# Performance work log

Hardware: AMD Instinct MI355X
Metric: run time of the kernel (lower is better)

## Reference

```python
import jax, jax.numpy as jnp
import numpy as np


def crf_log_likelihood(logits, tags, mask, transitions, start_trans, end_trans):
    """AllenNLP-style linear-chain CRF log-likelihood, summed over the batch.
    logits: [B,T,K] float, tags: [B,T] int, mask: [B,T] float (1=valid).
    include_start_end_transitions=True.
    """
    B, T, K = logits.shape
    lt = jnp.transpose(logits, (1, 0, 2))          # [T,B,K]
    mt = jnp.transpose(mask, (1, 0))               # [T,B]
    tt = jnp.transpose(tags, (1, 0))               # [T,B]

    # ---- partition function (forward algorithm) ----
    alpha0 = start_trans + lt[0]                   # [B,K]

    def part_step(alpha, xs):
        emit, m = xs                               # emit [B,K], m [B]
        # inner[b,i,j] = alpha[b,i] + transitions[i,j] + emit[b,j]
        inner = alpha[:, :, None] + emit[:, None, :] + transitions[None, :, :]
        new_alpha = jax.nn.logsumexp(inner, axis=1)
        alpha = new_alpha * m[:, None] + alpha * (1.0 - m[:, None])
        return alpha, None

    alpha, _ = jax.lax.scan(part_step, alpha0, (lt[1:], mt[1:]))
    log_denominator = jax.nn.logsumexp(alpha + end_trans, axis=1)  # [B]

    # ---- joint (gold-path) score ----
    score0 = start_trans[tt[0]]                    # [B]

    def joint_step(score, xs):
        cur, nxt, emit, m_cur, m_nxt = xs
        trans_s = transitions[cur, nxt]                                   # [B]
        emit_s = jnp.take_along_axis(emit, cur[:, None], axis=1)[:, 0]    # [B]
        return score + trans_s * m_nxt + emit_s * m_cur, None

    score, _ = jax.lax.scan(joint_step, score0,
                            (tt[:-1], tt[1:], lt[:-1], mt[:-1], mt[1:]))
    last_idx = (jnp.sum(mt, axis=0) - 1.0).astype(jnp.int32)              # [B]
    last_tags = tt[last_idx, jnp.arange(B)]                               # [B]
    last_emit = jnp.take_along_axis(lt[-1], last_tags[:, None], axis=1)[:, 0]
    score = score + end_trans[last_tags] + last_emit * mt[-1]
    return jnp.sum(score - log_denominator)


def setup_inputs() -> dict:
    key = jax.random.key(0)
    ks = jax.random.split(key, 6)
    B, T, D, K = 64, 512, 768, 21
    vectors = jax.random.normal(ks[0], (B, T, D), dtype=jnp.float32)
    targets = jax.random.randint(ks[1], (B, T), 0, K, dtype=jnp.int32)
    mask = jnp.ones((B, T), dtype=jnp.int32)
    # Linear(input_dim, n_classes)
    W = jax.random.normal(ks[2], (K, D), dtype=jnp.float32) * (1.0 / np.sqrt(D))
    b = jax.random.normal(ks[3], (K,), dtype=jnp.float32) * 0.01
    transitions = jax.random.normal(ks[4], (K, K), dtype=jnp.float32) * 0.1
    se = jax.random.normal(ks[5], (2, K), dtype=jnp.float32) * 0.1
    return {"vectors": vectors, "targets": targets, "mask": mask,
            "W": W, "b": b, "transitions": transitions,
            "start_trans": se[0], "end_trans": se[1]}


def reference(vectors, targets, mask, W, b, transitions, start_trans, end_trans):
    logits = jnp.einsum('btd,kd->btk', vectors, W) + b     # proj
    maskf = mask.astype(logits.dtype)
    ll = crf_log_likelihood(logits, targets, maskf, transitions, start_trans, end_trans)
    loss = -ll / jnp.sum(maskf)
    return loss, logits
```

## Files before the change

### kernel.cpp

```cpp
#include <hip/hip_runtime.h>

#define B_ 64
#define T_ 512
#define D_ 768
#define K_ 21
#define NCHUNK 32
#define CLEN 16
#define GSTRIDE 448
#define LOG21 3.0445224377234229965f

__global__ __launch_bounds__(512) void proj_kernel(
    const float* __restrict__ A,
    const float* __restrict__ W,
    const float* __restrict__ bias,
    float* __restrict__ out)
{
    __shared__ float Wl[K_ * D_];
    const int tid = threadIdx.x;
    {
        const float4* Wg = (const float4*)W;
        float4* Ws = (float4*)Wl;
        for (int i = tid; i < K_ * D_ / 4; i += 512) Ws[i] = Wg[i];
    }
    __syncthreads();

    const int m = tid & 15;
    const size_t row = (size_t)blockIdx.x * 32 + (tid >> 4);
    const float4* __restrict__ Arow = (const float4*)(A + row * D_);
    const float4* __restrict__ Wl4 = (const float4*)Wl;

    float acc[K_];
    #pragma unroll
    for (int k = 0; k < K_; ++k) acc[k] = 0.0f;

    #pragma unroll 4
    for (int i = 0; i < 12; ++i) {
        const float4 a = Arow[m + 16 * i];
        #pragma unroll
        for (int k = 0; k < K_; ++k) {
            const float4 w = Wl4[k * 192 + m + 16 * i];
            acc[k] = fmaf(a.x, w.x, fmaf(a.y, w.y, fmaf(a.z, w.z, fmaf(a.w, w.w, acc[k]))));
        }
    }

    #pragma unroll
    for (int k = 0; k < K_; ++k) {
        float v = acc[k];
        v += __shfl_xor(v, 1, 64);
        v += __shfl_xor(v, 2, 64);
        v += __shfl_xor(v, 4, 64);
        v += __shfl_xor(v, 8, 64);
        acc[k] = v;
    }

    float* o = out + 1 + row * K_;
    #pragma unroll
    for (int k = 0; k < K_; ++k) {
        if (m == (k & 15)) o[k] = acc[k] + bias[k];
    }
}

__global__ __launch_bounds__(64) void chunk_kernel(
    const float* __restrict__ outF,
    const int*   __restrict__ mask,
    const float* __restrict__ trans,
    float* __restrict__ G,
    float* __restrict__ SC)
{
    __shared__ float M0[441], M1[441];
    __shared__ float sET[441];
    __shared__ float em[CLEN * K_];
    __shared__ float smx[CLEN];
    __shared__ int   smask[CLEN];

    const int c = blockIdx.x;
    const int b = blockIdx.y;
    const int lane = threadIdx.x;
    const int t0 = c * CLEN + 1;
    const int nst = min(CLEN, T_ - t0);
    const int i_ = lane / 3;
    const int jg = lane - i_ * 3;
    const bool act = lane < 63;

    const float* lg = outF + 1 + (size_t)b * T_ * K_;
    for (int idx = lane; idx < nst * K_; idx += 64) em[idx] = lg[t0 * K_ + idx];
    if (lane < nst) smask[lane] = mask[b * T_ + t0 + lane];
    for (int idx = lane; idx < 441; idx += 64) {
        M0[idx] = (idx % 22 == 0) ? 1.0f : 0.0f;
        sET[idx] = __expf(trans[idx]);
    }
    __syncthreads();

    if (lane < nst) {
        float mx = -1e30f;
        for (int j = 0; j < K_; ++j) mx = fmaxf(mx, em[lane * K_ + j]);
        smx[lane] = mx;
    }
    __syncthreads();
    for (int idx = lane; idx < nst * K_; idx += 64)
        em[idx] = __expf(em[idx] - smx[idx / K_]) * (1.0f / 21.0f);

    float ETc[K_ * 7];
    if (act) {
        #pragma unroll
        for (int mm = 0; mm < K_; ++mm) {
            #pragma unroll
            for (int q = 0; q < 7; ++q)
                ETc[mm * 7 + q] = sET[mm * K_ + jg * 7 + q];
        }
    }
    __syncthreads();

    int cur = 0;
    for (int s = 0; s < nst; ++s) {
        if (smask[s] != 0) {
            const float* Mr = cur ? M1 : M0;
            float*       Mw = cur ? M0 : M1;
            float facc[7] = {0.f,0.f,0.f,0.f,0.f,0.f,0.f};
            if (act) {
                #pragma unroll
                for (int mm = 0; mm < K_; ++mm) {
                    const float lm = Mr[i_ * K_ + mm];
                    #pragma unroll
                    for (int q = 0; q < 7; ++q)
                        facc[q] = fmaf(lm, ETc[mm * 7 + q], facc[q]);
                }
            }
            __syncthreads();
            if (act) {
                #pragma unroll
                for (int q = 0; q < 7; ++q)
                    Mw[i_ * K_ + jg * 7 + q] = facc[q] * em[s * K_ + jg * 7 + q];
            }
            __syncthreads();
            cur ^= 1;
        }
    }

    float* Gc = G + (size_t)(b * NCHUNK + c) * GSTRIDE;
    const float* Mf = cur ? M1 : M0;
    for (int idx = lane; idx < 441; idx += 64) Gc[idx] = Mf[idx];
    if (lane == 0) {
        float sc = 0.0f;
        for (int s = 0; s < nst; ++s)
            if (smask[s] != 0) sc += smx[s] + LOG21;
        SC[b * NCHUNK + c] = sc;
    }
}

__global__ __launch_bounds__(64) void scan_kernel(
    const float* __restrict__ outF,
    const int*   __restrict__ tags,
    const int*   __restrict__ mask,
    const float* __restrict__ trans,
    const float* __restrict__ startT,
    const float* __restrict__ endT,
    const float* __restrict__ G,
    const float* __restrict__ SC,
    float* __restrict__ ll,
    float* __restrict__ msum)
{
    __shared__ float sG[2][GSTRIDE];
    __shared__ float sv[24];
    __shared__ float sm[T_];
    __shared__ int   st[T_];
    const int b = blockIdx.x;
    const int lane = threadIdx.x;
    const int jc = min(lane, K_ - 1);
    const float* lg = outF + 1 + (size_t)b * T_ * K_;
    const float* Gb = G + (size_t)b * NCHUNK * GSTRIDE;

    for (int t = lane; t < T_; t += 64) {
        sm[t] = (float)mask[b * T_ + t];
        st[t] = tags[b * T_ + t];
    }
    const float scv = (lane < NCHUNK) ? SC[b * NCHUNK + lane] : 0.0f;

    {
        const float4* Gf4 = (const float4*)Gb;
        float4* dst = (float4*)sG[0];
        dst[lane] = Gf4[lane];
        if (lane < 48) dst[lane + 64] = Gf4[lane + 64];
    }

    float val = (lane < K_) ? startT[lane] + lg[lane] : -1e30f;
    float mx = val;
    #pragma unroll
    for (int off = 32; off >= 1; off >>= 1) mx = fmaxf(mx, __shfl_xor(mx, off, 64));
    float v = (lane < K_) ? __expf(val - mx) : 0.0f;
    float C = mx;

    for (int c = 0; c < NCHUNK; ++c) {
        if (lane < K_) sv[lane] = v;
        __syncthreads();

        float4 p0, p1;
        const bool have = (c + 1) < NCHUNK;
        if (have) {
            const float4* Gf4 = (const float4*)(Gb + (size_t)(c + 1) * GSTRIDE);
            p0 = Gf4[lane];
            if (lane < 48) p1 = Gf4[lane + 64];
        }

        const float* Gc = sG[c & 1];
        float a0 = 0.f, a1 = 0.f, a2 = 0.f;
        #pragma unroll
        for (int i = 0; i < K_; i += 3) {
            a0 = fmaf(sv[i],     Gc[i * K_ + jc],       a0);
            a1 = fmaf(sv[i + 1], Gc[(i + 1) * K_ + jc], a1);
            a2 = fmaf(sv[i + 2], Gc[(i + 2) * K_ + jc], a2);
        }
        const float s = a0 + a1 + a2;
        C += __shfl(scv, c, 64);
        float m2 = (lane < K_) ? s : 0.0f;
        #pragma unroll
        for (int off = 32; off >= 1; off >>= 1) m2 = fmaxf(m2, __shfl_xor(m2, off, 64));
        v = (lane < K_) ? s / m2 : 0.0f;
        C += __logf(m2);

        if (have) {
            float4* dst = (float4*)sG[(c + 1) & 1];
            dst[lane] = p0;
            if (lane < 48) dst[lane + 64] = p1;
        }
        __syncthreads();
    }

    float term = (lane < K_) ? v * __expf(endT[lane]) : 0.0f;
    #pragma unroll
    for (int off = 32; off >= 1; off >>= 1) term += __shfl_xor(term, off, 64);
    const float logZ = C + __logf(term);

    float sc = 0.0f, ms = 0.0f;
    for (int t = lane; t < T_; t += 64) {
        const float mt = sm[t];
        ms += mt;
        if (t < T_ - 1) {
            const int ct = st[t], nt2 = st[t + 1];
            sc += trans[ct * K_ + nt2] * sm[t + 1] + lg[t * K_ + ct] * mt;
        }
    }
    #pragma unroll
    for (int off = 32; off >= 1; off >>= 1) {
        sc += __shfl_xor(sc, off, 64);
        ms += __shfl_xor(ms, off, 64);
    }
    if (lane == 0) {
        const int lastIdx = (int)ms - 1;
        const int lastTag = st[lastIdx];
        sc += startT[st[0]] + endT[lastTag] + lg[(T_ - 1) * K_ + lastTag] * sm[T_ - 1];
        ll[b]   = sc - logZ;
        msum[b] = ms;
    }
}

__global__ __launch_bounds__(64) void crf_kernel(
    const float* __restrict__ outF,
    const int*   __restrict__ tags,
    const int*   __restrict__ mask,
    const float* __restrict__ trans,
    const float* __restrict__ startT,
    const float* __restrict__ endT,
    float* __restrict__ ws)
{
    __shared__ float se[T_ * K_];
    __shared__ float sm[T_];
    __shared__ int   st[T_];
    const int b = blockIdx.x;
    const int lane = threadIdx.x;

    const float* lg = outF + 1 + (size_t)b * T_ * K_;
    for (int i = lane; i < T_ * K_; i += 64) se[i] = lg[i];
    for (int t = lane; t < T_; t += 64) {
        sm[t] = (float)mask[b * T_ + t];
        st[t] = tags[b * T_ + t];
    }
    __syncthreads();

    const int jc = lane < K_ ? lane : K_ - 1;
    float ET[K_];
    #pragma unroll
    for (int i = 0; i < K_; ++i) ET[i] = __expf(trans[i * K_ + jc]);

    float a0   = startT[jc] + se[jc];
    float r0   = __shfl(a0, 0, 64);
    float aRel = a0 - r0;
    float C    = r0;

    for (int t = 1; t < T_; ++t) {
        if (sm[t] != 0.0f) {
            float e = __expf(aRel);
            float s = 0.0f;
            #pragma unroll
            for (int i = 0; i < K_; ++i)
                s = fmaf(__shfl(e, i, 64), ET[i], s);
            float raw = __logf(s) + se[t * K_ + jc];
            float rr  = __shfl(raw, 0, 64);
            aRel = raw - rr;
            C   += rr;
        }
    }

    float contrib = (lane < K_) ? __expf(aRel + endT[jc]) : 0.0f;
    #pragma unroll
    for (int off = 32; off >= 1; off >>= 1) contrib += __shfl_xor(contrib, off, 64);
    const float logZ = C + __logf(contrib);

    float sc = 0.0f, ms = 0.0f;
    for (int t = lane; t < T_; t += 64) {
        const float mt = sm[t];
        ms += mt;
        if (t < T_ - 1) {
            const int ct = st[t], nt2 = st[t + 1];
            sc += trans[ct * K_ + nt2] * sm[t + 1] + se[t * K_ + ct] * mt;
        }
    }
    #pragma unroll
    for (int off = 32; off >= 1; off >>= 1) {
        sc += __shfl_xor(sc, off, 64);
        ms += __shfl_xor(ms, off, 64);
    }
    if (lane == 0) {
        const int lastIdx = (int)ms - 1;
        const int lastTag = st[lastIdx];
        sc += startT[st[0]] + endT[lastTag] + se[(T_ - 1) * K_ + lastTag] * sm[T_ - 1];
        ws[b]      = sc - logZ;
        ws[B_ + b] = ms;
    }
}

__global__ __launch_bounds__(64) void fin_kernel(
    const float* __restrict__ ll, const float* __restrict__ msum,
    float* __restrict__ outF)
{
    const int lane = threadIdx.x;
    float l = ll[lane];
    float m = msum[lane];
    #pragma unroll
    for (int off = 32; off >= 1; off >>= 1) {
        l += __shfl_xor(l, off, 64);
        m += __shfl_xor(m, off, 64);
    }
    if (lane == 0) outF[0] = -l / m;
}

extern "C" void kernel_launch(void* const* d_in, const int* in_sizes, int n_in,
                              void* d_out, int out_size, void* d_ws, size_t ws_size,
                              hipStream_t stream) {
    const float* A     = (const float*)d_in[0];
    const int*   tags  = (const int*)  d_in[1];
    const int*   mask  = (const int*)  d_in[2];
    const float* W     = (const float*)d_in[3];
    const float* bias  = (const float*)d_in[4];
    const float* trans = (const float*)d_in[5];
    const float* stT   = (const float*)d_in[6];
    const float* enT   = (const float*)d_in[7];
    float* outF = (float*)d_out;
    float* ws   = (float*)d_ws;

    proj_kernel<<<1024, 512, 0, stream>>>(A, W, bias, outF);

    const size_t gFloats  = (size_t)B_ * NCHUNK * GSTRIDE;
    const size_t scOff    = gFloats;
    const size_t llOff    = gFloats + (size_t)B_ * NCHUNK;
    const size_t msOff    = llOff + B_;
    const size_t needBytes = (msOff + B_) * sizeof(float);

    if (ws_size >= needBytes) {
        float* G   = ws;
        float* SC  = ws + scOff;
        float* llp = ws + llOff;
        float* msv = ws + msOff;
        chunk_kernel<<<dim3(NCHUNK, B_), 64, 0, stream>>>(outF, mask, trans, G, SC);
        scan_kernel<<<B_, 64, 0, stream>>>(outF, tags, mask, trans, stT, enT, G, SC, llp, msv);
        fin_kernel<<<1, 64, 0, stream>>>(llp, msv, outF);
    } else {
        crf_kernel<<<B_, 64, 0, stream>>>(outF, tags, mask, trans, stT, enT, ws);
        fin_kernel<<<1, 64, 0, stream>>>(ws, ws + B_, outF);
    }
}
```

Baseline: 218.3 us.

## Use fp16 MFMA for projection and preload all chunk matrices in scan

The projection kernel now computes the 32768x21 logits with fp16 MFMA 16x16x32 instructions. Each wave handles 16 rows and reads A and W directly from global memory, converting to half on the fly, instead of staging W in LDS and doing scalar FMAs with shuffle reductions. Separately, the scan kernel loads all 32 chunk transfer matrices into shared memory up front rather than double-buffering one chunk per iteration. This takes global loads off the serial scan loop. The cost is reduced logit precision from fp16 rounding of the inputs and a much larger LDS footprint per scan block.

```diff
diff --git a/kernel.cpp b/kernel.cpp
--- a/kernel.cpp
+++ b/kernel.cpp
@@ -9,54 +9,61 @@
 #define GSTRIDE 448
 #define LOG21 3.0445224377234229965f
 
-__global__ __launch_bounds__(512) void proj_kernel(
+using f16x8 = __attribute__((ext_vector_type(8))) _Float16;
+using f32x4 = __attribute__((ext_vector_type(4))) float;
+
+__global__ __launch_bounds__(256) void proj_kernel(
     const float* __restrict__ A,
     const float* __restrict__ W,
     const float* __restrict__ bias,
     float* __restrict__ out)
 {
-    __shared__ float Wl[K_ * D_];
-    const int tid = threadIdx.x;
+    const int lane = threadIdx.x & 63;
+    const int wave = threadIdx.x >> 6;
+    const int row0 = (blockIdx.x * 4 + wave) * 16;
+    const int m = lane & 15;
+    const int kb = (lane >> 4) * 8;
+
+    const float* __restrict__ Ar  = A + (size_t)(row0 + m) * D_ + kb;
+    const float* __restrict__ Wr0 = W + (size_t)m * D_ + kb;
+    const int n1 = (16 + m < K_) ? 16 + m : K_ - 1;
+    const float* __restrict__ Wr1 = W + (size_t)n1 * D_ + kb;
+
+    f32x4 acc0 = {0.f, 0.f, 0.f, 0.f};
+    f32x4 acc1 = {0.f, 0.f, 0.f, 0.f};
+
+    #pragma unroll 8
+    for (int s = 0; s < 24; ++s) {
+        const float4 aL = *(const float4*)(Ar  + s * 32);
+        const float4 aH = *(const float4*)(Ar  + s * 32 + 4);
+        const float4 bL = *(const float4*)(Wr0 + s * 32);
+        const float4 bH = *(const float4*)(Wr0 + s * 32 + 4);
+        const float4 cL = *(const float4*)(Wr1 + s * 32);
+        const float4 cH = *(const float4*)(Wr1 + s * 32 + 4);
+        f16x8 af, bf, cf;
+        af[0]=(_Float16)aL.x; af[1]=(_Float16)aL.y; af[2]=(_Float16)aL.z; af[3]=(_Float16)aL.w;
+        af[4]=(_Float16)aH.x; af[5]=(_Float16)aH.y; af[6]=(_Float16)aH.z; af[7]=(_Float16)aH.w;
+        bf[0]=(_Float16)bL.x; bf[1]=(_Float16)bL.y; bf[2]=(_Float16)bL.z; bf[3]=(_Float16)bL.w;
+        bf[4]=(_Float16)bH.x; bf[5]=(_Float16)bH.y; bf[6]=(_Float16)bH.z; bf[7]=(_Float16)bH.w;
+        cf[0]=(_Float16)cL.x; cf[1]=(_Float16)cL.y; cf[2]=(_Float16)cL.z; cf[3]=(_Float16)cL.w;
+        cf[4]=(_Float16)cH.x; cf[5]=(_Float16)cH.y; cf[6]=(_Float16)cH.z; cf[7]=(_Float16)cH.w;
+        acc0 = __builtin_amdgcn_mfma_f32_16x16x32_f16(af, bf, acc0, 0, 0, 0);
+        acc1 = __builtin_amdgcn_mfma_f32_16x16x32_f16(af, cf, acc1, 0, 0, 0);
+    }
+
+    const int rbase = row0 + (lane >> 4) * 4;
     {
-        const float4* Wg = (const float4*)W;
-        float4* Ws = (float4*)Wl;
-        for (int i = tid; i < K_ * D_ / 4; i += 512) Ws[i] = Wg[i];
-    }
-    __syncthreads();
-
-    const int m = tid & 15;
-    const size_t row = (size_t)blockIdx.x * 32 + (tid >> 4);
-    const float4* __restrict__ Arow = (const float4*)(A + row * D_);
-    const float4* __restrict__ Wl4 = (const float4*)Wl;
-
-    float acc[K_];
-    #pragma unroll
-    for (int k = 0; k < K_; ++k) acc[k] = 0.0f;
-
-    #pragma unroll 4
-    for (int i = 0; i < 12; ++i) {
-        const float4 a = Arow[m + 16 * i];
-        #pragma unroll
-        for (int k = 0; k < K_; ++k) {
-            const float4 w = Wl4[k * 192 + m + 16 * i];
-            acc[k] = fmaf(a.x, w.x, fmaf(a.y, w.y, fmaf(a.z, w.z, fmaf(a.w, w.w, acc[k]))));
-        }
-    }
-
-    #pragma unroll
-    for (int k = 0; k < K_; ++k) {
-        float v = acc[k];
-        v += __shfl_xor(v, 1, 64);
-        v += __shfl_xor(v, 2, 64);
-        v += __shfl_xor(v, 4, 64);
-        v += __shfl_xor(v, 8, 64);
-        acc[k] = v;
-    }
-
-    float* o = out + 1 + row * K_;
-    #pragma unroll
-    for (int k = 0; k < K_; ++k) {
-        if (m == (k & 15)) o[k] = acc[k] + bias[k];
+        const float bb = bias[m];
+        float* o = out + 1 + (size_t)rbase * K_ + m;
+        #pragma unroll
+        for (int r = 0; r < 4; ++r) o[(size_t)r * K_] = acc0[r] + bb;
+    }
+    const int col2 = 16 + m;
+    if (col2 < K_) {
+        const float bb = bias[col2];
+        float* o = out + 1 + (size_t)rbase * K_ + col2;
+        #pragma unroll
+        for (int r = 0; r < 4; ++r) o[(size_t)r * K_] = acc1[r] + bb;
     }
 }
 
@@ -160,7 +167,7 @@
     float* __restrict__ ll,
     float* __restrict__ msum)
 {
-    __shared__ float sG[2][GSTRIDE];
+    __shared__ float sG[NCHUNK * GSTRIDE];
     __shared__ float sv[24];
     __shared__ float sm[T_];
     __shared__ int   st[T_];
@@ -170,39 +177,29 @@
     const float* lg = outF + 1 + (size_t)b * T_ * K_;
     const float* Gb = G + (size_t)b * NCHUNK * GSTRIDE;
 
+    {
+        const float4* Gf4 = (const float4*)Gb;
+        float4* dst = (float4*)sG;
+        for (int j = lane; j < NCHUNK * GSTRIDE / 4; j += 64) dst[j] = Gf4[j];
+    }
     for (int t = lane; t < T_; t += 64) {
         sm[t] = (float)mask[b * T_ + t];
         st[t] = tags[b * T_ + t];
     }
     const float scv = (lane < NCHUNK) ? SC[b * NCHUNK + lane] : 0.0f;
 
-    {
-        const float4* Gf4 = (const float4*)Gb;
-        float4* dst = (float4*)sG[0];
-        dst[lane] = Gf4[lane];
-        if (lane < 48) dst[lane + 64] = Gf4[lane + 64];
-    }
-
     float val = (lane < K_) ? startT[lane] + lg[lane] : -1e30f;
     float mx = val;
     #pragma unroll
     for (int off = 32; off >= 1; off >>= 1) mx = fmaxf(mx, __shfl_xor(mx, off, 64));
     float v = (lane < K_) ? __expf(val - mx) : 0.0f;
     float C = mx;
+    __syncthreads();
 
     for (int c = 0; c < NCHUNK; ++c) {
         if (lane < K_) sv[lane] = v;
         __syncthreads();
-
-        float4 p0, p1;
-        const bool have = (c + 1) < NCHUNK;
-        if (have) {
-            const float4* Gf4 = (const float4*)(Gb + (size_t)(c + 1) * GSTRIDE);
-            p0 = Gf4[lane];
-            if (lane < 48) p1 = Gf4[lane + 64];
-        }
-
-        const float* Gc = sG[c & 1];
+        const float* Gc = sG + c * GSTRIDE;
         float a0 = 0.f, a1 = 0.f, a2 = 0.f;
         #pragma unroll
         for (int i = 0; i < K_; i += 3) {
@@ -217,12 +214,6 @@
         for (int off = 32; off >= 1; off >>= 1) m2 = fmaxf(m2, __shfl_xor(m2, off, 64));
         v = (lane < K_) ? s / m2 : 0.0f;
         C += __logf(m2);
-
-        if (have) {
-            float4* dst = (float4*)sG[(c + 1) & 1];
-            dst[lane] = p0;
-            if (lane < 48) dst[lane + 64] = p1;
-        }
         __syncthreads();
     }
 
@@ -358,7 +349,7 @@
     float* outF = (float*)d_out;
     float* ws   = (float*)d_ws;
 
-    proj_kernel<<<1024, 512, 0, stream>>>(A, W, bias, outF);
+    proj_kernel<<<512, 256, 0, stream>>>(A, W, bias, outF);
 
     const size_t gFloats  = (size_t)B_ * NCHUNK * GSTRIDE;
     const size_t scOff    = gFloats;
```

After: 225.9 us. 1.03x slower.
